# Performance work log

Measured on AMD Instinct MI355X. Metric: run time of the kernel, lower is better.

## Reference

```python
import jax, jax.numpy as jnp
import numpy as np

BN_EPS = 1e-5


def conv_bn_relu(x, w, b, gamma, beta):
    # Conv2d(stride=2, padding=1) -> BatchNorm2d (training-mode batch stats) -> ReLU
    y = jax.lax.conv_general_dilated(
        x, w, window_strides=(2, 2), padding=((1, 1), (1, 1)),
        dimension_numbers=('NCHW', 'OIHW', 'NCHW')) + b[None, :, None, None]
    mu = y.mean(axis=(0, 2, 3))
    var = y.var(axis=(0, 2, 3))
    y = (y - mu[None, :, None, None]) * jax.lax.rsqrt(var + BN_EPS)[None, :, None, None]
    y = y * gamma[None, :, None, None] + beta[None, :, None, None]
    return jax.nn.relu(y)


def setup_inputs() -> dict:
    key = jax.random.key(0)
    ks = jax.random.split(key, 12)
    N, C, HW_IN = 32, 3, 64
    SD = 24           # stem_dim
    RQ = 128          # rnn_hidden_dim
    MD = 128          # module_dim
    FC = 1024         # classifier hidden
    NA = 2            # num answers
    D_PAIR = (SD + 2) * 2 + RQ  # 180
    s = 0.05
    return {
        'image':   jax.random.normal(ks[0], (N, C, HW_IN, HW_IN), jnp.float32),
        'ques':    jax.random.normal(ks[1], (N, RQ), jnp.float32),
        'conv1_w': jax.random.normal(ks[2], (SD, C, 3, 3), jnp.float32) * s,
        'conv1_b': jnp.zeros((SD,), jnp.float32),
        'bn1_g':   jnp.ones((SD,), jnp.float32),
        'bn1_b':   jnp.zeros((SD,), jnp.float32),
        'conv2_w': jax.random.normal(ks[3], (SD, SD, 3, 3), jnp.float32) * s,
        'conv2_b': jnp.zeros((SD,), jnp.float32),
        'bn2_g':   jnp.ones((SD,), jnp.float32),
        'bn2_b':   jnp.zeros((SD,), jnp.float32),
        'w_rel':   jax.random.normal(ks[4], (D_PAIR, MD), jnp.float32) * s,
        'b_rel':   jnp.zeros((MD,), jnp.float32),
        'w_fc1':   jax.random.normal(ks[5], (MD, FC), jnp.float32) * s,
        'b_fc1':   jnp.zeros((FC,), jnp.float32),
        'w_fc2':   jax.random.normal(ks[6], (FC, NA), jnp.float32) * s,
        'b_fc2':   jnp.zeros((NA,), jnp.float32),
    }


def reference(image, ques, conv1_w, conv1_b, bn1_g, bn1_b,
              conv2_w, conv2_b, bn2_g, bn2_b,
              w_rel, b_rel, w_fc1, b_fc1, w_fc2, b_fc2):
    f = conv_bn_relu(image, conv1_w, conv1_b, bn1_g, bn1_b)
    f = conv_bn_relu(f, conv2_w, conv2_b, bn2_g, bn2_b)
    N, F, H, W = f.shape
    HW = H * W
    flat = f.reshape(N, F, HW).transpose(0, 2, 1)      # (N, HW, F)

    # coordinate grid exactly as in the torch code (stacked over (W, H))
    xs = jnp.linspace(-1.0, 1.0, W)
    ys = jnp.linspace(-1.0, 1.0, H)
    xv = jnp.repeat(xs[:, None], H, axis=1)            # (W, H)
    yv = jnp.repeat(ys[None, :], W, axis=0)            # (W, H)
    coords = jnp.stack([xv, yv], axis=2).reshape(-1, 2)  # (HW, 2)

    fc = jnp.concatenate(
        [flat, jnp.broadcast_to(coords[None], (N, HW, 2))], axis=2)  # (N, HW, F+2)
    D = F + 2

    # relation layer is a single Linear over cat([x_i, x_j, ques]) followed by
    # a sum over ALL (HW)^2 pairs. Because the layer is linear, the pair sum
    # decomposes exactly:
    #   sum_{a,b} (fc[b] Wi + fc[a] Wj + q Wq + b_rel)
    # = HW * (sum_p fc[p]) (Wi + Wj) + HW^2 * (q Wq + b_rel)
    Wi, Wj, Wq = w_rel[:D], w_rel[D:2 * D], w_rel[2 * D:]
    s = fc.sum(axis=1)                                  # (N, D)
    hw = jnp.asarray(HW, fc.dtype)
    relations = hw * (s @ (Wi + Wj)) + (hw * hw) * (ques @ Wq + b_rel)  # (N, 128)

    # ---- classifier: Linear -> ReLU -> Linear ----
    h = jax.nn.relu(relations @ w_fc1 + b_fc1)
    out = h @ w_fc2 + b_fc2                             # (N, num_answers)
    return out
```

## Files before the change

### kernel.cpp

```cpp
#include <hip/hip_runtime.h>
#include <math.h>


#define MAGIC 0x13579BDFu
#define AGENT __HIP_MEMORY_SCOPE_AGENT
#define PITCH 40
#define NROWS 33
#define CHSZ (PITCH * NROWS)
#define C_OUT 24

__device__ __forceinline__ float aload(const float* p) {
  return __hip_atomic_load(p, __ATOMIC_RELAXED, AGENT);
}
__device__ __forceinline__ void astore(float* p, float v) {
  __hip_atomic_store(p, v, __ATOMIC_RELAXED, AGENT);
}
__device__ __forceinline__ unsigned aloadu(const unsigned* p) {
  return __hip_atomic_load(p, __ATOMIC_RELAXED, AGENT);
}
__device__ __forceinline__ void astoreu(unsigned* p, unsigned v) {
  __hip_atomic_store(p, v, __ATOMIC_RELAXED, AGENT);
}
__device__ __forceinline__ void waitflag(const unsigned* f) {
  while (__hip_atomic_load(f, __ATOMIC_RELAXED, AGENT) != MAGIC)
    __builtin_amdgcn_s_sleep(1);
}

__global__ __launch_bounds__(1024) void fused_wide(
    const float* __restrict__ img, const float* __restrict__ ques,
    const float* __restrict__ c1w, const float* __restrict__ c1b,
    const float* __restrict__ g1,  const float* __restrict__ bt1,
    const float* __restrict__ c2w, const float* __restrict__ c2b,
    const float* __restrict__ g2,  const float* __restrict__ bt2,
    const float* __restrict__ w_rel, const float* __restrict__ b_rel,
    const float* __restrict__ w_fc1, const float* __restrict__ b_fc1,
    const float* __restrict__ w_fc2, const float* __restrict__ b_fc2,
    float* __restrict__ out,
    unsigned* __restrict__ flags1, unsigned* __restrict__ flags2,
    unsigned* __restrict__ flags3, unsigned* __restrict__ flags4,
    float* __restrict__ p1, float* __restrict__ p2,
    float* __restrict__ ssum, float* __restrict__ pairs,
    unsigned* __restrict__ y1g) {
  const int t = threadIdx.x;
  const int bid = blockIdx.x;
  const int lane = t & 63, wid = t >> 6;
  const int n = bid & 31;
  const int seg = bid >> 5;
  const int cobase = seg * 3;

  __shared__ __align__(16) unsigned short y1u[24 * CHSZ];
  __align__(16) __shared__ float red[5120];
  __shared__ float s_a[C_OUT], s_b[C_OUT];
  __shared__ float a2[3], b2[3];
  __shared__ float chS[64], chS2[64];
  __shared__ float qpart[1024];
  __shared__ float qfull[128];
  __shared__ float s_s[26];
  __shared__ float s_coef[128];
  unsigned* lds32 = (unsigned*)y1u;

  {
    const int oh = t >> 5, ow = t & 31;
    float win[27];
    #pragma unroll
    for (int ci = 0; ci < 3; ci++)
      #pragma unroll
      for (int kh = 0; kh < 3; kh++) {
        int ih = oh * 2 - 1 + kh;
        #pragma unroll
        for (int kw = 0; kw < 3; kw++) {
          int iw = ow * 2 - 1 + kw;
          win[ci * 9 + kh * 3 + kw] =
              (ih >= 0 && iw >= 0) ? img[(n * 3 + ci) * 4096 + ih * 64 + iw] : 0.f;
        }
      }
    unsigned x16[3]; float xb[3];
    #pragma unroll
    for (int j = 0; j < 3; j++) {
      const int co = cobase + j;
      float acc = c1b[co];
      #pragma unroll
      for (int q = 0; q < 27; q++) acc += win[q] * c1w[co * 27 + q];
      unsigned bits = __float_as_uint(acc);
      unsigned rr = (bits + 0x7FFFu + ((bits >> 16) & 1u)) >> 16;
      x16[j] = rr;
      xb[j] = __uint_as_float(rr << 16);
    }
    const unsigned base = ((unsigned)(n * 24 + cobase) * 32 + oh) * 17;
    #pragma unroll
    for (int j = 0; j < 3; j++) {
      unsigned up = (unsigned)__shfl_down((int)x16[j], 1, 64);
      const unsigned rb = base + (unsigned)j * 544;
      if (ow & 1) {
        unsigned hi = (ow == 31) ? 0u : up;
        astoreu(&y1g[rb + ((unsigned)(ow + 1) >> 1)], x16[j] | (hi << 16));
      } else if (ow == 0) {
        astoreu(&y1g[rb], x16[j] << 16);
      }
    }
    #pragma unroll
    for (int j = 0; j < 3; j++) {
      float s = xb[j], s2 = xb[j] * xb[j];
      #pragma unroll
      for (int off = 32; off > 0; off >>= 1) {
        s += __shfl_down(s, off, 64);
        s2 += __shfl_down(s2, off, 64);
      }
      if (lane == 0) { chS[j * 16 + wid] = s; chS2[j * 16 + wid] = s2; }
    }
  }
  __syncthreads();
  if (t < 3) {
    float s = 0.f, s2 = 0.f;
    #pragma unroll
    for (int i = 0; i < 16; i++) { s += chS[t * 16 + i]; s2 += chS2[t * 16 + i]; }
    astore(&p1[(cobase + t) * 32 + n], s);
    astore(&p1[768 + (cobase + t) * 32 + n], s2);
  }
  __syncthreads();
  if (t == 0)
    __hip_atomic_store(&flags1[bid], MAGIC, __ATOMIC_RELEASE, AGENT);

  {
    float pf = 0.f;
    if (t < 512) pf += w_fc1[(t >> 2) * 1024 + seg * 128 + (t & 3) * 32];
    if (t < 720) pf += w_rel[t * 32];
    if (t < 8)   pf += w_fc2[seg * 256 + t * 32];
    if (t < 4)   pf += b_fc1[seg * 128 + t * 32];
    asm volatile("" :: "v"(pf));
  }

  if (t < 8 && t != seg) waitflag(&flags1[t * 32 + n]);
  __syncthreads();
  {
    const unsigned* yg = y1g + n * 13056;
    for (int i = t; i < 13056; i += 1024) {
      unsigned v = aloadu(yg + i);
      int co = i / 544;
      int rem = i - co * 544;
      int row = rem / 17;
      int c = rem - row * 17;
      lds32[co * 660 + (row + 1) * 20 + c] = v;
    }
  }
  if (t < 256) waitflag(&flags1[t]);
  __syncthreads();
  if (t < 768) {
    int ch = t >> 5, j = t & 31;
    float s = aload(&p1[ch * 32 + j]);
    float s2 = aload(&p1[768 + ch * 32 + j]);
    #pragma unroll
    for (int off = 16; off > 0; off >>= 1) {
      s += __shfl_down(s, off, 32);
      s2 += __shfl_down(s2, off, 32);
    }
    if (j == 0) {
      float mu = s * (1.f / 32768.f);
      float var = s2 * (1.f / 32768.f) - mu * mu;
      float a = rsqrtf(var + 1e-5f) * g1[ch];
      s_a[ch] = a;
      s_b[ch] = bt1[ch] - mu * a;
    }
  }
  __syncthreads();

  const int px = t & 255;
  const int slot = t >> 8;
  {
    const int o2h = px >> 4, o2w = px & 15;
    float accq[3] = {0.f, 0.f, 0.f};
    const int ci0 = slot * 6;
    #pragma unroll
    for (int cc = 0; cc < 6; cc++) {
      const int ci = ci0 + cc;
      const float a1 = s_a[ci], b1 = s_b[ci];
      const unsigned* chp = lds32 + ci * 660;
      #pragma unroll
      for (int kh = 0; kh < 3; kh++) {
        const int row = o2h * 2 + kh;
        const unsigned* pr = chp + row * 20;
        unsigned w0 = pr[o2w];
        unsigned w1 = pr[o2w + 1];
        float x0 = __uint_as_float(w0 << 16);
        float x1 = __uint_as_float(w0 & 0xffff0000u);
        float x2 = __uint_as_float(w1 << 16);
        x0 = fmaxf(fmaf(x0, a1, b1), 0.f);
        x1 = fmaxf(fmaf(x1, a1, b1), 0.f);
        x2 = fmaxf(fmaf(x2, a1, b1), 0.f);
        if (row == 0) { x0 = 0.f; x1 = 0.f; x2 = 0.f; }
        if (o2w == 0) x0 = 0.f;
        #pragma unroll
        for (int j = 0; j < 3; j++) {
          const float* wp = c2w + ((cobase + j) * C_OUT + ci) * 9 + kh * 3;
          accq[j] = fmaf(x0, wp[0], fmaf(x1, wp[1], fmaf(x2, wp[2], accq[j])));
        }
      }
    }
    #pragma unroll
    for (int j = 0; j < 3; j++) red[(slot * 256 + px) * 5 + j] = accq[j];
  }
  __syncthreads();
  float acc2 = 0.f;
  const int j2 = t >> 8;
  if (t < 768) {
    acc2 = c2b[cobase + j2];
    #pragma unroll
    for (int s = 0; s < 4; s++) acc2 += red[(s * 256 + px) * 5 + j2];
    float s = acc2, s2 = acc2 * acc2;
    #pragma unroll
    for (int off = 32; off > 0; off >>= 1) {
      s += __shfl_down(s, off, 64);
      s2 += __shfl_down(s2, off, 64);
    }
    if (lane == 0) { chS[j2 * 4 + (wid & 3)] = s; chS2[j2 * 4 + (wid & 3)] = s2; }
  }
  __syncthreads();
  if (t < 3) {
    float s = chS[t * 4] + chS[t * 4 + 1] + chS[t * 4 + 2] + chS[t * 4 + 3];
    float s2 = chS2[t * 4] + chS2[t * 4 + 1] + chS2[t * 4 + 2] + chS2[t * 4 + 3];
    astore(&p2[(cobase + t) * 32 + n], s);
    astore(&p2[768 + (cobase + t) * 32 + n], s2);
  }
  __syncthreads();
  if (t == 0)
    __hip_atomic_store(&flags2[bid], MAGIC, __ATOMIC_RELEASE, AGENT);

  {
    int m = t & 127, g = t >> 7;
    const float* qv = ques + n * 128;
    float q = 0.f;
    for (int k = g * 16; k < g * 16 + 16; k++)
      q += qv[k] * w_rel[(52 + k) * 128 + m];
    qpart[t] = q;
  }
  __syncthreads();
  if (t < 128) {
    float q = b_rel[t];
    #pragma unroll
    for (int g = 0; g < 8; g++) q += qpart[g * 128 + t];
    qfull[t] = 65536.f * q;
  }

  if (t < 256) waitflag(&flags2[t]);
  __syncthreads();
  if (t < 96) {
    int j = t >> 5, l = t & 31;
    float s = aload(&p2[(cobase + j) * 32 + l]);
    float s2 = aload(&p2[768 + (cobase + j) * 32 + l]);
    #pragma unroll
    for (int off = 16; off > 0; off >>= 1) {
      s += __shfl_down(s, off, 32);
      s2 += __shfl_down(s2, off, 32);
    }
    if (l == 0) {
      float mu = s * (1.f / 8192.f);
      float var = s2 * (1.f / 8192.f) - mu * mu;
      float a = rsqrtf(var + 1e-5f) * g2[cobase + j];
      a2[j] = a;
      b2[j] = bt2[cobase + j] - mu * a;
    }
  }
  __syncthreads();

  if (t < 768) {
    float v = acc2 * a2[j2] + b2[j2];
    v = v > 0.f ? v : 0.f;
    #pragma unroll
    for (int off = 32; off > 0; off >>= 1) v += __shfl_down(v, off, 64);
    if (lane == 0) chS[j2 * 4 + (wid & 3)] = v;
  }
  __syncthreads();
  if (t < 3)
    astore(&ssum[n * C_OUT + cobase + t],
           chS[t * 4] + chS[t * 4 + 1] + chS[t * 4 + 2] + chS[t * 4 + 3]);
  __syncthreads();
  if (t == 0)
    __hip_atomic_store(&flags3[bid], MAGIC, __ATOMIC_RELEASE, AGENT);

  if (t < 8 && t != seg) waitflag(&flags3[t * 32 + n]);
  __syncthreads();
  if (t < C_OUT) s_s[t] = aload(&ssum[n * C_OUT + t]);
  if (t == 24 || t == 25) {
    float cs = 0.f;
    for (int i = 0; i < 16; i++) cs += -1.f + 2.f * (float)i / 15.f;
    s_s[t] = 16.f * cs;
  }
  __syncthreads();
  {
    int col = t & 127, g = t >> 7;
    float p = 0.f;
    #pragma unroll
    for (int dd = 0; dd < 4; dd++) {
      int d = g + dd * 8;
      if (d < 26)
        p += s_s[d] * (w_rel[d * 128 + col] + w_rel[(26 + d) * 128 + col]);
    }
    qpart[t] = p;
  }
  __syncthreads();
  if (t < 128) {
    float sterm = 0.f;
    #pragma unroll
    for (int g = 0; g < 8; g++) sterm += qpart[g * 128 + t];
    s_coef[t] = qfull[t] + 256.f * sterm;
  }
  __syncthreads();

  {
    const int gi = t & 31, ms = t >> 5;
    const float4* wp = (const float4*)w_fc1 + seg * 32 + gi;
    float4 a4 = make_float4(0.f, 0.f, 0.f, 0.f);
    #pragma unroll
    for (int k = 0; k < 4; k++) {
      int m = ms * 4 + k;
      float c = s_coef[m];
      float4 w = wp[m * 256];
      a4.x = fmaf(c, w.x, a4.x); a4.y = fmaf(c, w.y, a4.y);
      a4.z = fmaf(c, w.z, a4.z); a4.w = fmaf(c, w.w, a4.w);
    }
    red[(gi * 4 + 0) * 33 + ms] = a4.x;
    red[(gi * 4 + 1) * 33 + ms] = a4.y;
    red[(gi * 4 + 2) * 33 + ms] = a4.z;
    red[(gi * 4 + 3) * 33 + ms] = a4.w;
  }
  __syncthreads();
  float a0 = 0.f, a1v = 0.f;
  if (t < 128) {
    float h = b_fc1[seg * 128 + t];
    #pragma unroll
    for (int ms = 0; ms < 32; ms++) h += red[t * 33 + ms];
    h = h > 0.f ? h : 0.f;
    a0 = h * w_fc2[(seg * 128 + t) * 2];
    a1v = h * w_fc2[(seg * 128 + t) * 2 + 1];
  }
  {
    #pragma unroll
    for (int off = 32; off > 0; off >>= 1) {
      a0 += __shfl_down(a0, off, 64);
      a1v += __shfl_down(a1v, off, 64);
    }
    if (t < 128 && lane == 0) { chS[wid] = a0; chS2[wid] = a1v; }
  }
  __syncthreads();
  if (t == 0) {
    float b0 = chS[0] + chS[1], b1 = chS2[0] + chS2[1];
    if (seg != 0) {
      astore(&pairs[n * 16 + seg * 2 + 0], b0);
      astore(&pairs[n * 16 + seg * 2 + 1], b1);
      __hip_atomic_store(&flags4[bid], MAGIC, __ATOMIC_RELEASE, AGENT);
    } else {
      s_coef[0] = b0; s_coef[1] = b1;
    }
  }
  if (seg != 0) return;

  if (t >= 1 && t < 8) waitflag(&flags4[t * 32 + n]);
  __syncthreads();
  if (t == 0) {
    float b0 = s_coef[0], b1 = s_coef[1];
    #pragma unroll
    for (int i = 1; i < 8; i++) {
      b0 += aload(&pairs[n * 16 + i * 2 + 0]);
      b1 += aload(&pairs[n * 16 + i * 2 + 1]);
    }
    out[n * 2 + 0] = b0 + b_fc2[0];
    out[n * 2 + 1] = b1 + b_fc2[1];
  }
}

__global__ __launch_bounds__(1024) void fused_kernel_r3(
    const float* __restrict__ img, const float* __restrict__ ques,
    const float* __restrict__ c1w, const float* __restrict__ c1b,
    const float* __restrict__ g1,  const float* __restrict__ bt1,
    const float* __restrict__ c2w, const float* __restrict__ c2b,
    const float* __restrict__ g2,  const float* __restrict__ bt2,
    const float* __restrict__ w_rel, const float* __restrict__ b_rel,
    const float* __restrict__ w_fc1, const float* __restrict__ b_fc1,
    const float* __restrict__ w_fc2, const float* __restrict__ b_fc2,
    float* __restrict__ out,
    unsigned* __restrict__ flags1, unsigned* __restrict__ flags2,
    unsigned* __restrict__ flags3, unsigned* __restrict__ flags4,
    float* __restrict__ p1, float* __restrict__ p2,
    float* __restrict__ ssum, float* __restrict__ pairs) {
  const int t = threadIdx.x;
  const int bid = blockIdx.x;
  const int lane = t & 63, wid = t >> 6;
  const int n = bid & 31;
  const int r = bid >> 5;
  const int g0 = r * 43 - (r == 5 ? 1 : 0);
  const int gcnt = (r < 4) ? 43 : 42;

  __shared__ unsigned short y1u[24 * CHSZ];
  __align__(16) __shared__ float red[5120];
  __shared__ float s_a[C_OUT], s_b[C_OUT];
  __shared__ float a2[4], b2[4];
  __shared__ float chS[16], chS2[16];
  __shared__ float qpart[1024];
  __shared__ float qfull[128];
  __shared__ float s_s[26];
  __shared__ float s_coef[128];

  if (t < 24 * PITCH) {
    int ch = t / PITCH;
    y1u[ch * CHSZ + (t - ch * PITCH)] = 0;
  }
  if (t < 768)
    y1u[(t >> 5) * CHSZ + ((t & 31) + 1) * PITCH] = 0;

  {
    int oh = t >> 5, ow = t & 31;
    float win[27];
    #pragma unroll
    for (int ci = 0; ci < 3; ci++)
      #pragma unroll
      for (int kh = 0; kh < 3; kh++) {
        int ih = oh * 2 - 1 + kh;
        #pragma unroll
        for (int kw = 0; kw < 3; kw++) {
          int iw = ow * 2 - 1 + kw;
          win[ci * 9 + kh * 3 + kw] =
              (ih >= 0 && iw >= 0) ? img[(n * 3 + ci) * 4096 + ih * 64 + iw] : 0.f;
        }
      }
    #pragma unroll
    for (int co = 0; co < C_OUT; co++) {
      float acc = c1b[co];
      #pragma unroll
      for (int q = 0; q < 27; q++) acc += win[q] * c1w[co * 27 + q];
      unsigned bits = __float_as_uint(acc);
      unsigned rr = (bits + 0x7FFFu + ((bits >> 16) & 1u)) >> 16;
      y1u[co * CHSZ + (oh + 1) * PITCH + (ow + 1)] = (unsigned short)rr;
    }
  }
  __syncthreads();

  if (r == 0) {
    if (t < 768) {
      int ch = t >> 5, l = t & 31;
      float s = 0.f, s2 = 0.f;
      #pragma unroll
      for (int i = 0; i < 32; i++) {
        float x = __uint_as_float(
            (unsigned)y1u[ch * CHSZ + (i + 1) * PITCH + (l + 1)] << 16);
        s += x; s2 += x * x;
      }
      #pragma unroll
      for (int off = 16; off > 0; off >>= 1) {
        s += __shfl_down(s, off, 32);
        s2 += __shfl_down(s2, off, 32);
      }
      if (l == 0) {
        astore(&p1[ch * 32 + n], s);
        astore(&p1[768 + ch * 32 + n], s2);
      }
    }
    __syncthreads();
    if (t == 0)
      __hip_atomic_store(&flags1[n], MAGIC, __ATOMIC_RELEASE, AGENT);
  }

  {
    float pf = 0.f;
    {
      int row = t >> 3, l = t & 7;
      int col = g0 * 4 + l * 32;
      col = col < 1024 ? col : 1023;
      pf += w_fc1[row * 1024 + col];
    }
    if (t < 720) pf += w_rel[t * 32];
    if (t < 64)  pf += w_fc2[t * 32];
    if (t < 32)  pf += b_fc1[t * 32];
    asm volatile("" :: "v"(pf));
  }

  if (t < 32) waitflag(&flags1[t]);
  __syncthreads();
  if (t < 768) {
    int ch = t >> 5, j = t & 31;
    float s = aload(&p1[ch * 32 + j]);
    float s2 = aload(&p1[768 + ch * 32 + j]);
    #pragma unroll
    for (int off = 16; off > 0; off >>= 1) {
      s += __shfl_down(s, off, 32);
      s2 += __shfl_down(s2, off, 32);
    }
    if (j == 0) {
      float mu = s * (1.f / 32768.f);
      float var = s2 * (1.f / 32768.f) - mu * mu;
      float a = rsqrtf(var + 1e-5f) * g1[ch];
      s_a[ch] = a;
      s_b[ch] = bt1[ch] - mu * a;
    }
  }
  __syncthreads();

  const int px = t & 255;
  const int slot = t >> 8;
  const int co2 = r * 4 + slot;
  float acc2;
  {
    const int o2h = px >> 4, o2w = px & 15;
    float accq[4] = {0.f, 0.f, 0.f, 0.f};
    const int ci0 = slot * 6;
    #pragma unroll
    for (int cc = 0; cc < 6; cc++) {
      const int ci = ci0 + cc;
      const float a1 = s_a[ci], b1 = s_b[ci];
      const unsigned* chp = (const unsigned*)(y1u + ci * CHSZ);
      #pragma unroll
      for (int kh = 0; kh < 3; kh++) {
        const int row = o2h * 2 + kh;
        const unsigned* pr = chp + row * (PITCH / 2);
        unsigned w0 = pr[o2w];
        unsigned w1 = pr[o2w + 1];
        float x0 = __uint_as_float(w0 << 16);
        float x1 = __uint_as_float(w0 & 0xffff0000u);
        float x2 = __uint_as_float(w1 << 16);
        x0 = fmaxf(fmaf(x0, a1, b1), 0.f);
        x1 = fmaxf(fmaf(x1, a1, b1), 0.f);
        x2 = fmaxf(fmaf(x2, a1, b1), 0.f);
        if (row == 0) { x0 = 0.f; x1 = 0.f; x2 = 0.f; }
        if (o2w == 0) x0 = 0.f;
        #pragma unroll
        for (int co = 0; co < 4; co++) {
          const float* wp = c2w + ((r * 4 + co) * C_OUT + ci) * 9 + kh * 3;
          accq[co] = fmaf(x0, wp[0], accq[co]);
          accq[co] = fmaf(x1, wp[1], accq[co]);
          accq[co] = fmaf(x2, wp[2], accq[co]);
        }
      }
    }
    #pragma unroll
    for (int q = 0; q < 4; q++) red[(slot * 256 + px) * 5 + q] = accq[q];
  }
  __syncthreads();
  {
    acc2 = c2b[co2];
    #pragma unroll
    for (int s = 0; s < 4; s++) acc2 += red[(s * 256 + px) * 5 + slot];
  }
  {
    float s = acc2, s2 = acc2 * acc2;
    #pragma unroll
    for (int off = 32; off > 0; off >>= 1) {
      s += __shfl_down(s, off, 64);
      s2 += __shfl_down(s2, off, 64);
    }
    if (lane == 0) { chS[slot * 4 + (wid & 3)] = s; chS2[slot * 4 + (wid & 3)] = s2; }
  }
  __syncthreads();
  if (t < 4) {
    float s = chS[t * 4] + chS[t * 4 + 1] + chS[t * 4 + 2] + chS[t * 4 + 3];
    float s2 = chS2[t * 4] + chS2[t * 4 + 1] + chS2[t * 4 + 2] + chS2[t * 4 + 3];
    astore(&p2[(r * 4 + t) * 32 + n], s);
    astore(&p2[768 + (r * 4 + t) * 32 + n], s2);
  }
  __syncthreads();
  if (t == 0)
    __hip_atomic_store(&flags2[bid], MAGIC, __ATOMIC_RELEASE, AGENT);

  {
    int m = t & 127, g = t >> 7;
    const float* qv = ques + n * 128;
    float q = 0.f;
    for (int k = g * 16; k < g * 16 + 16; k++)
      q += qv[k] * w_rel[(52 + k) * 128 + m];
    qpart[t] = q;
  }
  __syncthreads();
  if (t < 128) {
    float q = b_rel[t];
    #pragma unroll
    for (int g = 0; g < 8; g++) q += qpart[g * 128 + t];
    qfull[t] = 65536.f * q;
  }

  if (t < 32) waitflag(&flags2[r * 32 + t]);
  __syncthreads();
  if (t < 128) {
    int c4 = t >> 5, j = t & 31;
    float s = aload(&p2[(r * 4 + c4) * 32 + j]);
    float s2 = aload(&p2[768 + (r * 4 + c4) * 32 + j]);
    #pragma unroll
    for (int off = 16; off > 0; off >>= 1) {
      s += __shfl_down(s, off, 32);
      s2 += __shfl_down(s2, off, 32);
    }
    if (j == 0) {
      float mu = s * (1.f / 8192.f);
      float var = s2 * (1.f / 8192.f) - mu * mu;
      float a = rsqrtf(var + 1e-5f) * g2[r * 4 + c4];
      a2[c4] = a;
      b2[c4] = bt2[r * 4 + c4] - mu * a;
    }
  }
  __syncthreads();

  {
    float v = acc2 * a2[slot] + b2[slot];
    v = v > 0.f ? v : 0.f;
    #pragma unroll
    for (int off = 32; off > 0; off >>= 1) v += __shfl_down(v, off, 64);
    if (lane == 0) chS[slot * 4 + (wid & 3)] = v;
  }
  __syncthreads();
  if (t < 4)
    astore(&ssum[n * C_OUT + r * 4 + t],
           chS[t * 4] + chS[t * 4 + 1] + chS[t * 4 + 2] + chS[t * 4 + 3]);
  __syncthreads();
  if (t == 0)
    __hip_atomic_store(&flags3[bid], MAGIC, __ATOMIC_RELEASE, AGENT);

  if (t < 6 && t != r) waitflag(&flags3[t * 32 + n]);
  __syncthreads();
  if (t < C_OUT) s_s[t] = aload(&ssum[n * C_OUT + t]);
  if (t == 24 || t == 25) {
    float cs = 0.f;
    for (int i = 0; i < 16; i++) cs += -1.f + 2.f * (float)i / 15.f;
    s_s[t] = 16.f * cs;
  }
  __syncthreads();

  {
    int col = t & 127, g = t >> 7;
    float p = 0.f;
    #pragma unroll
    for (int dd = 0; dd < 4; dd++) {
      int d = g + dd * 8;
      if (d < 26)
        p += s_s[d] * (w_rel[d * 128 + col] + w_rel[(26 + d) * 128 + col]);
    }
    qpart[t] = p;
  }
  __syncthreads();
  if (t < 128) {
    float sterm = 0.f;
    #pragma unroll
    for (int g = 0; g < 8; g++) sterm += qpart[g * 128 + t];
    s_coef[t] = qfull[t] + 256.f * sterm;
  }
  __syncthreads();

  {
    const int gi = lane, mseg = wid;
    if (gi < gcnt) {
      const float4* wp = (const float4*)w_fc1 + (g0 + gi);
      float4 acc = make_float4(0.f, 0.f, 0.f, 0.f);
      #pragma unroll
      for (int k = 0; k < 8; k++) {
        int m = mseg * 8 + k;
        float c = s_coef[m];
        float4 w = wp[m * 256];
        acc.x += c * w.x; acc.y += c * w.y; acc.z += c * w.z; acc.w += c * w.w;
      }
      ((float4*)red)[mseg * 43 + gi] = acc;
    }
  }
  __syncthreads();
  float a0 = 0.f, a1 = 0.f;
  if (t < gcnt * 4) {
    const int gcol = g0 * 4 + t;
    float h = b_fc1[gcol];
    #pragma unroll
    for (int mseg = 0; mseg < 16; mseg++) h += red[mseg * 172 + t];
    h = h > 0.f ? h : 0.f;
    a0 = h * w_fc2[2 * gcol];
    a1 = h * w_fc2[2 * gcol + 1];
  }
  __syncthreads();
  {
    #pragma unroll
    for (int off = 32; off > 0; off >>= 1) {
      a0 += __shfl_down(a0, off, 64);
      a1 += __shfl_down(a1, off, 64);
    }
    if (lane == 0) { chS[wid] = a0; chS2[wid] = a1; }
  }
  __syncthreads();
  if (t == 0) {
    float b0 = 0.f, b1v = 0.f;
    #pragma unroll
    for (int i = 0; i < 16; i++) { b0 += chS[i]; b1v += chS2[i]; }
    if (r != 0) {
      astore(&pairs[n * 12 + r * 2 + 0], b0);
      astore(&pairs[n * 12 + r * 2 + 1], b1v);
      __hip_atomic_store(&flags4[bid], MAGIC, __ATOMIC_RELEASE, AGENT);
    } else {
      chS[0] = b0; chS2[0] = b1v;
    }
  }
  if (r != 0) return;

  if (t >= 1 && t < 6) waitflag(&flags4[t * 32 + n]);
  __syncthreads();
  if (t == 0) {
    float b0 = chS[0], b1v = chS2[0];
    #pragma unroll
    for (int i = 1; i < 6; i++) {
      b0 += aload(&pairs[n * 12 + i * 2 + 0]);
      b1v += aload(&pairs[n * 12 + i * 2 + 1]);
    }
    out[n * 2 + 0] = b0 + b_fc2[0];
    out[n * 2 + 1] = b1v + b_fc2[1];
  }
}

extern "C" void kernel_launch(void* const* d_in, const int* in_sizes, int n_in,
                              void* d_out, int out_size, void* d_ws, size_t ws_size,
                              hipStream_t stream) {
  const float* image   = (const float*)d_in[0];
  const float* ques    = (const float*)d_in[1];
  const float* conv1_w = (const float*)d_in[2];
  const float* conv1_b = (const float*)d_in[3];
  const float* bn1_g   = (const float*)d_in[4];
  const float* bn1_b   = (const float*)d_in[5];
  const float* conv2_w = (const float*)d_in[6];
  const float* conv2_b = (const float*)d_in[7];
  const float* bn2_g   = (const float*)d_in[8];
  const float* bn2_b   = (const float*)d_in[9];
  const float* w_rel   = (const float*)d_in[10];
  const float* b_rel   = (const float*)d_in[11];
  const float* w_fc1   = (const float*)d_in[12];
  const float* b_fc1   = (const float*)d_in[13];
  const float* w_fc2   = (const float*)d_in[14];
  const float* b_fc2   = (const float*)d_in[15];
  float* out = (float*)d_out;

  const size_t WIDE_WORDS = 1024 + 1536 + 1536 + 768 + 512 + 417792;
  if (ws_size >= WIDE_WORDS * 4) {
    unsigned* flags1 = (unsigned*)d_ws;
    unsigned* flags2 = flags1 + 256;
    unsigned* flags3 = flags2 + 256;
    unsigned* flags4 = flags3 + 256;
    float* p1    = (float*)(flags4 + 256);
    float* p2    = p1 + 1536;
    float* ssum  = p2 + 1536;
    float* pairs = ssum + 768;
    unsigned* y1g = (unsigned*)(pairs + 512);
    fused_wide<<<256, 1024, 0, stream>>>(
        image, ques, conv1_w, conv1_b, bn1_g, bn1_b, conv2_w, conv2_b,
        bn2_g, bn2_b, w_rel, b_rel, w_fc1, b_fc1, w_fc2, b_fc2,
        out, flags1, flags2, flags3, flags4, p1, p2, ssum, pairs, y1g);
  } else {
    unsigned* flags1 = (unsigned*)d_ws;
    unsigned* flags2 = flags1 + 32;
    unsigned* flags3 = flags2 + 192;
    unsigned* flags4 = flags3 + 192;
    float* p1    = (float*)d_ws + 608;
    float* p2    = p1 + 1536;
    float* ssum  = p2 + 1536;
    float* pairs = ssum + 768;
    fused_kernel_r3<<<192, 1024, 0, stream>>>(
        image, ques, conv1_w, conv1_b, bn1_g, bn1_b, conv2_w, conv2_b,
        bn2_g, bn2_b, w_rel, b_rel, w_fc1, b_fc1, w_fc2, b_fc2,
        out, flags1, flags2, flags3, flags4, p1, p2, ssum, pairs);
  }
}
```

Baseline: 122.4 us.

## Split persistent flag-synchronized kernel into three launches with kernel-boundary barriers

Replaces the single 256-block kernel that used global spin-wait flags for cross-block BatchNorm statistics with three launches: conv1, conv2 (which now writes a bf16 conv2 output buffer), and a 32-block tail that computes BN2, the relation sum and the classifier per sample. Kernel boundaries act as grid-wide barriers, so the atomic flag polling, relaxed atomic loads and stores, and the cross-segment partial-sum exchange for the classifier go away. In exchange it adds two launch gaps and an extra global round trip for the conv2 activations. The tail also runs on only 32 blocks, each doing the full FC1 for one sample.

Measured after the change: 108.7 us. 1.13x faster.

```diff
diff --git a/kernel.cpp b/kernel.cpp
--- a/kernel.cpp
+++ b/kernel.cpp
@@ -15,112 +15,83 @@
 __device__ __forceinline__ void astore(float* p, float v) {
   __hip_atomic_store(p, v, __ATOMIC_RELAXED, AGENT);
 }
-__device__ __forceinline__ unsigned aloadu(const unsigned* p) {
-  return __hip_atomic_load(p, __ATOMIC_RELAXED, AGENT);
-}
-__device__ __forceinline__ void astoreu(unsigned* p, unsigned v) {
-  __hip_atomic_store(p, v, __ATOMIC_RELAXED, AGENT);
-}
 __device__ __forceinline__ void waitflag(const unsigned* f) {
   while (__hip_atomic_load(f, __ATOMIC_RELAXED, AGENT) != MAGIC)
     __builtin_amdgcn_s_sleep(1);
 }
-
-__global__ __launch_bounds__(1024) void fused_wide(
-    const float* __restrict__ img, const float* __restrict__ ques,
-    const float* __restrict__ c1w, const float* __restrict__ c1b,
-    const float* __restrict__ g1,  const float* __restrict__ bt1,
-    const float* __restrict__ c2w, const float* __restrict__ c2b,
-    const float* __restrict__ g2,  const float* __restrict__ bt2,
-    const float* __restrict__ w_rel, const float* __restrict__ b_rel,
-    const float* __restrict__ w_fc1, const float* __restrict__ b_fc1,
-    const float* __restrict__ w_fc2, const float* __restrict__ b_fc2,
-    float* __restrict__ out,
-    unsigned* __restrict__ flags1, unsigned* __restrict__ flags2,
-    unsigned* __restrict__ flags3, unsigned* __restrict__ flags4,
-    float* __restrict__ p1, float* __restrict__ p2,
-    float* __restrict__ ssum, float* __restrict__ pairs,
-    unsigned* __restrict__ y1g) {
+__device__ __forceinline__ unsigned rne16(float f) {
+  unsigned bits = __float_as_uint(f);
+  return (bits + 0x7FFFu + ((bits >> 16) & 1u)) >> 16;
+}
+
+__global__ __launch_bounds__(1024) void k1_conv1(
+    const float* __restrict__ img, const float* __restrict__ c1w,
+    const float* __restrict__ c1b,
+    const float* __restrict__ w_fc1, const float* __restrict__ w_rel,
+    const float* __restrict__ w_fc2, const float* __restrict__ b_fc1,
+    float* __restrict__ p1, unsigned* __restrict__ y1g) {
   const int t = threadIdx.x;
   const int bid = blockIdx.x;
   const int lane = t & 63, wid = t >> 6;
   const int n = bid & 31;
   const int seg = bid >> 5;
   const int cobase = seg * 3;
-
-  __shared__ __align__(16) unsigned short y1u[24 * CHSZ];
-  __align__(16) __shared__ float red[5120];
-  __shared__ float s_a[C_OUT], s_b[C_OUT];
-  __shared__ float a2[3], b2[3];
   __shared__ float chS[64], chS2[64];
-  __shared__ float qpart[1024];
-  __shared__ float qfull[128];
-  __shared__ float s_s[26];
-  __shared__ float s_coef[128];
-  unsigned* lds32 = (unsigned*)y1u;
-
-  {
-    const int oh = t >> 5, ow = t & 31;
-    float win[27];
-    #pragma unroll
-    for (int ci = 0; ci < 3; ci++)
+
+  const int oh = t >> 5, ow = t & 31;
+  float win[27];
+  #pragma unroll
+  for (int ci = 0; ci < 3; ci++)
+    #pragma unroll
+    for (int kh = 0; kh < 3; kh++) {
+      int ih = oh * 2 - 1 + kh;
       #pragma unroll
-      for (int kh = 0; kh < 3; kh++) {
-        int ih = oh * 2 - 1 + kh;
-        #pragma unroll
-        for (int kw = 0; kw < 3; kw++) {
-          int iw = ow * 2 - 1 + kw;
-          win[ci * 9 + kh * 3 + kw] =
-              (ih >= 0 && iw >= 0) ? img[(n * 3 + ci) * 4096 + ih * 64 + iw] : 0.f;
-        }
+      for (int kw = 0; kw < 3; kw++) {
+        int iw = ow * 2 - 1 + kw;
+        win[ci * 9 + kh * 3 + kw] =
+            (ih >= 0 && iw >= 0) ? img[(n * 3 + ci) * 4096 + ih * 64 + iw] : 0.f;
       }
-    unsigned x16[3]; float xb[3];
-    #pragma unroll
-    for (int j = 0; j < 3; j++) {
-      const int co = cobase + j;
-      float acc = c1b[co];
-      #pragma unroll
-      for (int q = 0; q < 27; q++) acc += win[q] * c1w[co * 27 + q];
-      unsigned bits = __float_as_uint(acc);
-      unsigned rr = (bits + 0x7FFFu + ((bits >> 16) & 1u)) >> 16;
-      x16[j] = rr;
-      xb[j] = __uint_as_float(rr << 16);
-    }
-    const unsigned base = ((unsigned)(n * 24 + cobase) * 32 + oh) * 17;
-    #pragma unroll
-    for (int j = 0; j < 3; j++) {
-      unsigned up = (unsigned)__shfl_down((int)x16[j], 1, 64);
-      const unsigned rb = base + (unsigned)j * 544;
-      if (ow & 1) {
-        unsigned hi = (ow == 31) ? 0u : up;
-        astoreu(&y1g[rb + ((unsigned)(ow + 1) >> 1)], x16[j] | (hi << 16));
-      } else if (ow == 0) {
-        astoreu(&y1g[rb], x16[j] << 16);
-      }
-    }
-    #pragma unroll
-    for (int j = 0; j < 3; j++) {
-      float s = xb[j], s2 = xb[j] * xb[j];
-      #pragma unroll
-      for (int off = 32; off > 0; off >>= 1) {
-        s += __shfl_down(s, off, 64);
-        s2 += __shfl_down(s2, off, 64);
-      }
-      if (lane == 0) { chS[j * 16 + wid] = s; chS2[j * 16 + wid] = s2; }
-    }
+    }
+  unsigned x16[3]; float xb[3];
+  #pragma unroll
+  for (int j = 0; j < 3; j++) {
+    const int co = cobase + j;
+    float acc = c1b[co];
+    #pragma unroll
+    for (int q = 0; q < 27; q++) acc += win[q] * c1w[co * 27 + q];
+    x16[j] = rne16(acc);
+    xb[j] = __uint_as_float(x16[j] << 16);
+  }
+  const unsigned base = ((unsigned)(n * 24 + cobase) * 32 + oh) * 17;
+  #pragma unroll
+  for (int j = 0; j < 3; j++) {
+    unsigned up = (unsigned)__shfl_down((int)x16[j], 1, 64);
+    const unsigned rb = base + (unsigned)j * 544;
+    if (ow & 1) {
+      unsigned hi = (ow == 31) ? 0u : up;
+      y1g[rb + ((unsigned)(ow + 1) >> 1)] = x16[j] | (hi << 16);
+    } else if (ow == 0) {
+      y1g[rb] = x16[j] << 16;
+    }
+  }
+  #pragma unroll
+  for (int j = 0; j < 3; j++) {
+    float s = xb[j], s2 = xb[j] * xb[j];
+    #pragma unroll
+    for (int off = 32; off > 0; off >>= 1) {
+      s += __shfl_down(s, off, 64);
+      s2 += __shfl_down(s2, off, 64);
+    }
+    if (lane == 0) { chS[j * 16 + wid] = s; chS2[j * 16 + wid] = s2; }
   }
   __syncthreads();
   if (t < 3) {
     float s = 0.f, s2 = 0.f;
     #pragma unroll
     for (int i = 0; i < 16; i++) { s += chS[t * 16 + i]; s2 += chS2[t * 16 + i]; }
-    astore(&p1[(cobase + t) * 32 + n], s);
-    astore(&p1[768 + (cobase + t) * 32 + n], s2);
-  }
-  __syncthreads();
-  if (t == 0)
-    __hip_atomic_store(&flags1[bid], MAGIC, __ATOMIC_RELEASE, AGENT);
-
+    p1[(cobase + t) * 32 + n] = s;
+    p1[768 + (cobase + t) * 32 + n] = s2;
+  }
   {
     float pf = 0.f;
     if (t < 512) pf += w_fc1[(t >> 2) * 1024 + seg * 128 + (t & 3) * 32];
@@ -129,13 +100,30 @@
     if (t < 4)   pf += b_fc1[seg * 128 + t * 32];
     asm volatile("" :: "v"(pf));
   }
-
-  if (t < 8 && t != seg) waitflag(&flags1[t * 32 + n]);
-  __syncthreads();
+}
+
+__global__ __launch_bounds__(1024) void k2_conv2(
+    const float* __restrict__ g1, const float* __restrict__ bt1,
+    const float* __restrict__ c2w, const float* __restrict__ c2b,
+    const float* __restrict__ p1, const unsigned* __restrict__ y1g,
+    float* __restrict__ p2, unsigned short* __restrict__ y2g) {
+  const int t = threadIdx.x;
+  const int bid = blockIdx.x;
+  const int lane = t & 63, wid = t >> 6;
+  const int n = bid & 31;
+  const int seg = bid >> 5;
+  const int cobase = seg * 3;
+
+  __shared__ __align__(16) unsigned short y1u[24 * CHSZ];
+  __align__(16) __shared__ float red[5120];
+  __shared__ float s_a[C_OUT], s_b[C_OUT];
+  __shared__ float chS[64], chS2[64];
+  unsigned* lds32 = (unsigned*)y1u;
+
   {
     const unsigned* yg = y1g + n * 13056;
     for (int i = t; i < 13056; i += 1024) {
-      unsigned v = aloadu(yg + i);
+      unsigned v = yg[i];
       int co = i / 544;
       int rem = i - co * 544;
       int row = rem / 17;
@@ -143,12 +131,10 @@
       lds32[co * 660 + (row + 1) * 20 + c] = v;
     }
   }
-  if (t < 256) waitflag(&flags1[t]);
-  __syncthreads();
   if (t < 768) {
     int ch = t >> 5, j = t & 31;
-    float s = aload(&p1[ch * 32 + j]);
-    float s2 = aload(&p1[768 + ch * 32 + j]);
+    float s = p1[ch * 32 + j];
+    float s2 = p1[768 + ch * 32 + j];
     #pragma unroll
     for (int off = 16; off > 0; off >>= 1) {
       s += __shfl_down(s, off, 32);
@@ -200,12 +186,12 @@
     for (int j = 0; j < 3; j++) red[(slot * 256 + px) * 5 + j] = accq[j];
   }
   __syncthreads();
-  float acc2 = 0.f;
   const int j2 = t >> 8;
   if (t < 768) {
-    acc2 = c2b[cobase + j2];
+    float acc2 = c2b[cobase + j2];
     #pragma unroll
     for (int s = 0; s < 4; s++) acc2 += red[(s * 256 + px) * 5 + j2];
+    y2g[(n * 24 + cobase + j2) * 256 + px] = (unsigned short)rne16(acc2);
     float s = acc2, s2 = acc2 * acc2;
     #pragma unroll
     for (int off = 32; off > 0; off >>= 1) {
@@ -218,76 +204,81 @@
   if (t < 3) {
     float s = chS[t * 4] + chS[t * 4 + 1] + chS[t * 4 + 2] + chS[t * 4 + 3];
     float s2 = chS2[t * 4] + chS2[t * 4 + 1] + chS2[t * 4 + 2] + chS2[t * 4 + 3];
-    astore(&p2[(cobase + t) * 32 + n], s);
-    astore(&p2[768 + (cobase + t) * 32 + n], s2);
-  }
-  __syncthreads();
-  if (t == 0)
-    __hip_atomic_store(&flags2[bid], MAGIC, __ATOMIC_RELEASE, AGENT);
-
-  {
-    int m = t & 127, g = t >> 7;
-    const float* qv = ques + n * 128;
-    float q = 0.f;
-    for (int k = g * 16; k < g * 16 + 16; k++)
-      q += qv[k] * w_rel[(52 + k) * 128 + m];
-    qpart[t] = q;
-  }
-  __syncthreads();
-  if (t < 128) {
-    float q = b_rel[t];
-    #pragma unroll
-    for (int g = 0; g < 8; g++) q += qpart[g * 128 + t];
-    qfull[t] = 65536.f * q;
-  }
-
-  if (t < 256) waitflag(&flags2[t]);
-  __syncthreads();
-  if (t < 96) {
-    int j = t >> 5, l = t & 31;
-    float s = aload(&p2[(cobase + j) * 32 + l]);
-    float s2 = aload(&p2[768 + (cobase + j) * 32 + l]);
+    p2[(cobase + t) * 32 + n] = s;
+    p2[768 + (cobase + t) * 32 + n] = s2;
+  }
+}
+
+__global__ __launch_bounds__(1024) void k3_tail(
+    const float* __restrict__ ques, const float* __restrict__ g2,
+    const float* __restrict__ bt2,
+    const float* __restrict__ w_rel, const float* __restrict__ b_rel,
+    const float* __restrict__ w_fc1, const float* __restrict__ b_fc1,
+    const float* __restrict__ w_fc2, const float* __restrict__ b_fc2,
+    const float* __restrict__ p2, const unsigned* __restrict__ y2g32,
+    float* __restrict__ out) {
+  const int t = threadIdx.x;
+  const int n = blockIdx.x;
+  const int lane = t & 63, wid = t >> 6;
+
+  __shared__ float s_a2[C_OUT], s_b2[C_OUT];
+  __shared__ float s_s[26];
+  __shared__ float qpart[1024], spart[1024];
+  __shared__ float s_coef[128];
+  __align__(16) __shared__ float red[4352];
+  __shared__ float chS[16], chS2[16];
+
+  if (t < 768) {
+    int ch = t >> 5, j = t & 31;
+    float s = p2[ch * 32 + j];
+    float s2 = p2[768 + ch * 32 + j];
     #pragma unroll
     for (int off = 16; off > 0; off >>= 1) {
       s += __shfl_down(s, off, 32);
       s2 += __shfl_down(s2, off, 32);
     }
-    if (l == 0) {
+    if (j == 0) {
       float mu = s * (1.f / 8192.f);
       float var = s2 * (1.f / 8192.f) - mu * mu;
-      float a = rsqrtf(var + 1e-5f) * g2[cobase + j];
-      a2[j] = a;
-      b2[j] = bt2[cobase + j] - mu * a;
+      float a = rsqrtf(var + 1e-5f) * g2[ch];
+      s_a2[ch] = a;
+      s_b2[ch] = bt2[ch] - mu * a;
     }
   }
   __syncthreads();
 
   if (t < 768) {
-    float v = acc2 * a2[j2] + b2[j2];
-    v = v > 0.f ? v : 0.f;
-    #pragma unroll
-    for (int off = 32; off > 0; off >>= 1) v += __shfl_down(v, off, 64);
-    if (lane == 0) chS[j2 * 4 + (wid & 3)] = v;
-  }
-  __syncthreads();
-  if (t < 3)
-    astore(&ssum[n * C_OUT + cobase + t],
-           chS[t * 4] + chS[t * 4 + 1] + chS[t * 4 + 2] + chS[t * 4 + 3]);
-  __syncthreads();
-  if (t == 0)
-    __hip_atomic_store(&flags3[bid], MAGIC, __ATOMIC_RELEASE, AGENT);
-
-  if (t < 8 && t != seg) waitflag(&flags3[t * 32 + n]);
-  __syncthreads();
-  if (t < C_OUT) s_s[t] = aload(&ssum[n * C_OUT + t]);
+    int ch = t >> 5, l = t & 31;
+    const uint4 w4 = ((const uint4*)(y2g32 + (size_t)(n * 24 + ch) * 128))[l];
+    const float a = s_a2[ch], b = s_b2[ch];
+    float v = 0.f;
+    const unsigned ws[4] = {w4.x, w4.y, w4.z, w4.w};
+    #pragma unroll
+    for (int q = 0; q < 4; q++) {
+      float xlo = __uint_as_float(ws[q] << 16);
+      float xhi = __uint_as_float(ws[q] & 0xffff0000u);
+      float vlo = fmaf(xlo, a, b); vlo = vlo > 0.f ? vlo : 0.f;
+      float vhi = fmaf(xhi, a, b); vhi = vhi > 0.f ? vhi : 0.f;
+      v += vlo + vhi;
+    }
+    #pragma unroll
+    for (int off = 16; off > 0; off >>= 1) v += __shfl_down(v, off, 32);
+    if (l == 0) s_s[ch] = v;
+  }
   if (t == 24 || t == 25) {
     float cs = 0.f;
     for (int i = 0; i < 16; i++) cs += -1.f + 2.f * (float)i / 15.f;
     s_s[t] = 16.f * cs;
   }
   __syncthreads();
+
   {
     int col = t & 127, g = t >> 7;
+    const float* qv = ques + n * 128;
+    float q = 0.f;
+    for (int k = g * 16; k < g * 16 + 16; k++)
+      q += qv[k] * w_rel[(52 + k) * 128 + col];
+    qpart[t] = q;
     float p = 0.f;
     #pragma unroll
     for (int dd = 0; dd < 4; dd++) {
@@ -295,43 +286,41 @@
       if (d < 26)
         p += s_s[d] * (w_rel[d * 128 + col] + w_rel[(26 + d) * 128 + col]);
     }
-    qpart[t] = p;
+    spart[t] = p;
   }
   __syncthreads();
   if (t < 128) {
-    float sterm = 0.f;
-    #pragma unroll
-    for (int g = 0; g < 8; g++) sterm += qpart[g * 128 + t];
-    s_coef[t] = qfull[t] + 256.f * sterm;
-  }
-  __syncthreads();
-
-  {
-    const int gi = t & 31, ms = t >> 5;
-    const float4* wp = (const float4*)w_fc1 + seg * 32 + gi;
+    float q = b_rel[t], st = 0.f;
+    #pragma unroll
+    for (int g = 0; g < 8; g++) { q += qpart[g * 128 + t]; st += spart[g * 128 + t]; }
+    s_coef[t] = 65536.f * q + 256.f * st;
+  }
+  __syncthreads();
+
+  {
+    const int cg = t & 255, mg = t >> 8;
+    const float4* wp = (const float4*)(w_fc1) + mg * 32 * 256 + cg;
     float4 a4 = make_float4(0.f, 0.f, 0.f, 0.f);
-    #pragma unroll
-    for (int k = 0; k < 4; k++) {
-      int m = ms * 4 + k;
-      float c = s_coef[m];
-      float4 w = wp[m * 256];
-      a4.x = fmaf(c, w.x, a4.x); a4.y = fmaf(c, w.y, a4.y);
-      a4.z = fmaf(c, w.z, a4.z); a4.w = fmaf(c, w.w, a4.w);
-    }
-    red[(gi * 4 + 0) * 33 + ms] = a4.x;
-    red[(gi * 4 + 1) * 33 + ms] = a4.y;
-    red[(gi * 4 + 2) * 33 + ms] = a4.z;
-    red[(gi * 4 + 3) * 33 + ms] = a4.w;
-  }
-  __syncthreads();
-  float a0 = 0.f, a1v = 0.f;
-  if (t < 128) {
-    float h = b_fc1[seg * 128 + t];
-    #pragma unroll
-    for (int ms = 0; ms < 32; ms++) h += red[t * 33 + ms];
+    #pragma unroll 8
+    for (int k = 0; k < 32; k++) {
+      float c = s_coef[mg * 32 + k];
+      float4 w = wp[k * 256];
+      a4.x += c * w.x; a4.y += c * w.y; a4.z += c * w.z; a4.w += c * w.w;
+    }
+    red[cg * 17 + mg * 4 + 0] = a4.x;
+    red[cg * 17 + mg * 4 + 1] = a4.y;
+    red[cg * 17 + mg * 4 + 2] = a4.z;
+    red[cg * 17 + mg * 4 + 3] = a4.w;
+  }
+  __syncthreads();
+  float a0, a1v;
+  {
+    float h = b_fc1[t];
+    #pragma unroll
+    for (int mg = 0; mg < 4; mg++) h += red[(t >> 2) * 17 + mg * 4 + (t & 3)];
     h = h > 0.f ? h : 0.f;
-    a0 = h * w_fc2[(seg * 128 + t) * 2];
-    a1v = h * w_fc2[(seg * 128 + t) * 2 + 1];
+    a0 = h * w_fc2[2 * t];
+    a1v = h * w_fc2[2 * t + 1];
   }
   {
     #pragma unroll
@@ -339,30 +328,13 @@
       a0 += __shfl_down(a0, off, 64);
       a1v += __shfl_down(a1v, off, 64);
     }
-    if (t < 128 && lane == 0) { chS[wid] = a0; chS2[wid] = a1v; }
+    if (lane == 0) { chS[wid] = a0; chS2[wid] = a1v; }
   }
   __syncthreads();
   if (t == 0) {
-    float b0 = chS[0] + chS[1], b1 = chS2[0] + chS2[1];
-    if (seg != 0) {
-      astore(&pairs[n * 16 + seg * 2 + 0], b0);
-      astore(&pairs[n * 16 + seg * 2 + 1], b1);
-      __hip_atomic_store(&flags4[bid], MAGIC, __ATOMIC_RELEASE, AGENT);
-    } else {
-      s_coef[0] = b0; s_coef[1] = b1;
-    }
-  }
-  if (seg != 0) return;
-
-  if (t >= 1 && t < 8) waitflag(&flags4[t * 32 + n]);
-  __syncthreads();
-  if (t == 0) {
-    float b0 = s_coef[0], b1 = s_coef[1];
-    #pragma unroll
-    for (int i = 1; i < 8; i++) {
-      b0 += aload(&pairs[n * 16 + i * 2 + 0]);
-      b1 += aload(&pairs[n * 16 + i * 2 + 1]);
-    }
+    float b0 = 0.f, b1 = 0.f;
+    #pragma unroll
+    for (int i = 0; i < 16; i++) { b0 += chS[i]; b1 += chS2[i]; }
     out[n * 2 + 0] = b0 + b_fc2[0];
     out[n * 2 + 1] = b1 + b_fc2[1];
   }
@@ -427,9 +399,7 @@
       float acc = c1b[co];
       #pragma unroll
       for (int q = 0; q < 27; q++) acc += win[q] * c1w[co * 27 + q];
-      unsigned bits = __float_as_uint(acc);
-      unsigned rr = (bits + 0x7FFFu + ((bits >> 16) & 1u)) >> 16;
-      y1u[co * CHSZ + (oh + 1) * PITCH + (ow + 1)] = (unsigned short)rr;
+      y1u[co * CHSZ + (oh + 1) * PITCH + (ow + 1)] = (unsigned short)rne16(acc);
     }
   }
   __syncthreads();
@@ -726,21 +696,19 @@
   const float* b_fc2   = (const float*)d_in[15];
   float* out = (float*)d_out;
 
-  const size_t WIDE_WORDS = 1024 + 1536 + 1536 + 768 + 512 + 417792;
-  if (ws_size >= WIDE_WORDS * 4) {
-    unsigned* flags1 = (unsigned*)d_ws;
-    unsigned* flags2 = flags1 + 256;
-    unsigned* flags3 = flags2 + 256;
-    unsigned* flags4 = flags3 + 256;
-    float* p1    = (float*)(flags4 + 256);
-    float* p2    = p1 + 1536;
-    float* ssum  = p2 + 1536;
-    float* pairs = ssum + 768;
-    unsigned* y1g = (unsigned*)(pairs + 512);
-    fused_wide<<<256, 1024, 0, stream>>>(
-        image, ques, conv1_w, conv1_b, bn1_g, bn1_b, conv2_w, conv2_b,
-        bn2_g, bn2_b, w_rel, b_rel, w_fc1, b_fc1, w_fc2, b_fc2,
-        out, flags1, flags2, flags3, flags4, p1, p2, ssum, pairs, y1g);
+  const size_t WORDS = 1536 + 1536 + 417792 + 98304;
+  if (ws_size >= WORDS * 4) {
+    float* p1 = (float*)d_ws;
+    float* p2 = p1 + 1536;
+    unsigned* y1g = (unsigned*)(p2 + 1536);
+    unsigned* y2g = y1g + 417792;
+    k1_conv1<<<256, 1024, 0, stream>>>(
+        image, conv1_w, conv1_b, w_fc1, w_rel, w_fc2, b_fc1, p1, y1g);
+    k2_conv2<<<256, 1024, 0, stream>>>(
+        bn1_g, bn1_b, conv2_w, conv2_b, p1, y1g, p2, (unsigned short*)y2g);
+    k3_tail<<<32, 1024, 0, stream>>>(
+        ques, bn2_g, bn2_b, w_rel, b_rel, w_fc1, b_fc1, w_fc2, b_fc2,
+        p2, y2g, out);
   } else {
     unsigned* flags1 = (unsigned*)d_ws;
     unsigned* flags2 = flags1 + 32;
```
